# Optimization experiments

Hardware: AMD Instinct MI355X
Metric: run time of the kernel (lower is better)

Reference implementation:

```python
import jax, jax.numpy as jnp
import numpy as np

HIDDEN = 1024
HEADS = 16
HEAD_DIM = HIDDEN // HEADS
EPS = 1e-6


def _layernorm(x, gamma, beta):
    mu = jnp.mean(x, axis=-1, keepdims=True)
    var = jnp.mean(jnp.square(x - mu), axis=-1, keepdims=True)
    return (x - mu) * jax.lax.rsqrt(var + EPS) * gamma + beta


def setup_inputs() -> dict:
    key = jax.random.key(0)
    ks = jax.random.split(key, 16)
    B, S, D = 2, 2048, HIDDEN
    s = 1.0 / np.sqrt(D)
    inp = {
        "x": jax.random.normal(ks[0], (B, S, D), dtype=jnp.float32),
        "Wq": jax.random.uniform(ks[1], (D, D), jnp.float32, -s, s),
        "bq": jnp.zeros((D,), jnp.float32),
        "Wk": jax.random.uniform(ks[2], (D, D), jnp.float32, -s, s),
        "bk": jnp.zeros((D,), jnp.float32),
        "Wv": jax.random.uniform(ks[3], (D, D), jnp.float32, -s, s),
        "bv": jnp.zeros((D,), jnp.float32),
        "Wo": jax.random.uniform(ks[4], (D, D), jnp.float32, -s, s),
        "bo": jnp.zeros((D,), jnp.float32),
        "g1": jnp.ones((D,), jnp.float32),
        "b1": jnp.zeros((D,), jnp.float32),
        "Wup": jax.random.uniform(ks[5], (D, 4 * D), jnp.float32, -s, s),
        "bup": jnp.zeros((4 * D,), jnp.float32),
        "Wdn": jax.random.uniform(ks[6], (4 * D, D), jnp.float32, -0.5 * s, 0.5 * s),
        "bdn": jnp.zeros((D,), jnp.float32),
        "g2": jnp.ones((D,), jnp.float32),
        "b2": jnp.zeros((D,), jnp.float32),
    }
    return inp


def _forward(x, Wq, bq, Wk, bk, Wv, bv, Wo, bo, g1, b1, Wup, bup, Wdn, bdn, g2, b2):
    B, S, D = x.shape
    H, Hd = HEADS, HEAD_DIM
    # projections -> (B, H, S, Hd)
    q = (x @ Wq + bq).reshape(B, S, H, Hd).transpose(0, 2, 1, 3)
    k = (x @ Wk + bk).reshape(B, S, H, Hd).transpose(0, 2, 1, 3)
    v = (x @ Wv + bv).reshape(B, S, H, Hd).transpose(0, 2, 1, 3)
    # full NxN scores (faithful to the source: explicit QK^T, mask, softmax, AV)
    scores = jnp.einsum("bhqd,bhkd->bhqk", q, k) / np.sqrt(Hd)
    causal = jnp.tril(jnp.ones((S, S), dtype=bool))  # (S, S)
    scores = jnp.where(causal, scores, jnp.float32(-1e20))
    attn = jax.nn.softmax(scores, axis=-1)
    # dropout is identity in eval mode
    mid = jnp.einsum("bhqk,bhkd->bqhd", attn, v).reshape(B, S, D)
    attn_out = mid @ Wo + bo
    x = _layernorm(x + attn_out, g1, b1)
    # FFN
    up = jax.nn.relu(x @ Wup + bup)
    down = up @ Wdn + bdn
    return _layernorm(x + down, g2, b2)


def reference(x, Wq, bq, Wk, bk, Wv, bv, Wo, bo, g1, b1, Wup, bup, Wdn, bdn, g2, b2):
    return _forward(x, Wq, bq, Wk, bk, Wv, bv, Wo, bo, g1, b1, Wup, bup, Wdn, bdn, g2, b2)
```

## Files before the change

kernel.cpp:

```cpp
#include <hip/hip_runtime.h>

#define D_MODEL 1024
#define D_FFN   4096
#define SEQ     2048
#define NROWS   4096
#define QKV_LD  3072
#define BKG     64

typedef __bf16 bf16x8 __attribute__((ext_vector_type(8)));
typedef float  floatx4 __attribute__((ext_vector_type(4)));

__device__ __forceinline__ unsigned short f2bf(float f) {
  unsigned int u = __float_as_uint(f);
  u += 0x7FFFu + ((u >> 16) & 1u);
  return (unsigned short)(u >> 16);
}

template <int C>
__device__ __forceinline__ float ror16(float x) {
  return __int_as_float(
      __builtin_amdgcn_mov_dpp(__float_as_int(x), 0x120 | C, 0xf, 0xf, true));
}

__device__ __forceinline__ void async16(const unsigned short* g, unsigned short* l) {
  __builtin_amdgcn_global_load_lds(
      (const __attribute__((address_space(1))) unsigned int*)g,
      (__attribute__((address_space(3))) unsigned int*)l, 16, 0, 0);
}

__global__ __launch_bounds__(256) void k_f32_to_bf16(
    const float* __restrict__ in, unsigned short* __restrict__ outp, long n) {
  long i = ((long)blockIdx.x * 256 + threadIdx.x) * 4;
  if (i >= n) return;
  float4 v = *(const float4*)(in + i);
  ushort4 o;
  o.x = f2bf(v.x); o.y = f2bf(v.y); o.z = f2bf(v.z); o.w = f2bf(v.w);
  *(ushort4*)(outp + i) = o;
}

__global__ __launch_bounds__(256) void k_transpose_bf16(
    const float* __restrict__ W, unsigned short* __restrict__ WT, int R, int C) {
  __shared__ float tile[32][33];
  int tx = threadIdx.x & 31, ty = threadIdx.x >> 5;
  long bx = (long)blockIdx.x * 32;
  long by = (long)blockIdx.y * 32;
  #pragma unroll
  for (int j = 0; j < 4; j++)
    tile[ty + j * 8][tx] = W[(by + ty + j * 8) * C + bx + tx];
  __syncthreads();
  #pragma unroll
  for (int j = 0; j < 4; j++)
    WT[(bx + ty + j * 8) * R + by + tx] = f2bf(tile[tx][ty + j * 8]);
}

__global__ __launch_bounds__(256) void k_transpose_sq(
    const float* __restrict__ Wq, const float* __restrict__ Wk,
    const float* __restrict__ Wv, const float* __restrict__ Wo,
    unsigned short* __restrict__ WqkvT, unsigned short* __restrict__ WoT) {
  __shared__ float tile[32][33];
  int z = blockIdx.z;
  const float* W = (z == 0) ? Wq : (z == 1) ? Wk : (z == 2) ? Wv : Wo;
  unsigned short* dst = (z < 3) ? (WqkvT + (size_t)z * D_MODEL * D_MODEL) : WoT;
  int tx = threadIdx.x & 31, ty = threadIdx.x >> 5;
  long bx = (long)blockIdx.x * 32;
  long by = (long)blockIdx.y * 32;
  #pragma unroll
  for (int j = 0; j < 4; j++)
    tile[ty + j * 8][tx] = W[(by + ty + j * 8) * D_MODEL + bx + tx];
  __syncthreads();
  #pragma unroll
  for (int j = 0; j < 4; j++)
    dst[(bx + ty + j * 8) * D_MODEL + by + tx] = f2bf(tile[tx][ty + j * 8]);
}

__global__ __launch_bounds__(256) void k_pack_bias(
    const float* __restrict__ bq, const float* __restrict__ bk,
    const float* __restrict__ bv, float* __restrict__ dst) {
  int i = blockIdx.x * 256 + threadIdx.x;
  if (i >= 3072) return;
  float v = (i < 1024) ? bq[i] : (i < 2048) ? bk[i - 1024] : bv[i - 2048];
  dst[i] = v;
}

__global__ __launch_bounds__(256) void k_transpose_v(
    const unsigned short* __restrict__ QKV, unsigned short* __restrict__ Vt) {
  __shared__ unsigned short tile[64][72];
  int r0 = blockIdx.x * 64;
  int c0 = blockIdx.y * 64;
  int tx = threadIdx.x & 15, ty = threadIdx.x >> 4;
  #pragma unroll
  for (int j = 0; j < 4; j++) {
    int r = ty + j * 16;
    *(ushort4*)&tile[r][tx * 4] =
        *(const ushort4*)(QKV + (long)(r0 + r) * QKV_LD + 2048 + c0 + tx * 4);
  }
  __syncthreads();
  #pragma unroll
  for (int j = 0; j < 4; j++) {
    int d = ty + j * 16;
    ushort4 o;
    o.x = tile[tx * 4 + 0][d];
    o.y = tile[tx * 4 + 1][d];
    o.z = tile[tx * 4 + 2][d];
    o.w = tile[tx * 4 + 3][d];
    *(ushort4*)(Vt + (long)(c0 + d) * NROWS + r0 + tx * 4) = o;
  }
}

__global__ __launch_bounds__(256) void k_gemm(
    const unsigned short* __restrict__ A,
    const unsigned short* __restrict__ Bt,
    const float* __restrict__ bias,
    void* __restrict__ Cp, int M, int N, int K, int flags) {
  __shared__ unsigned short As[128 * BKG];
  __shared__ unsigned short Bs[128 * BKG];
  int tid = threadIdx.x, lane = tid & 63, wave = tid >> 6;
  int quad = lane >> 4, l16 = lane & 15;
  int wm = (wave & 1) * 64, wn = (wave >> 1) * 64;
  long bm = (long)blockIdx.x * 128;
  long bn = (long)blockIdx.y * 128;
  int nz = gridDim.z, z = blockIdx.z;
  int Ks = K / nz;
  long zb = (long)z * Ks;

  const floatx4 fz = {0.f, 0.f, 0.f, 0.f};
  floatx4 acc[4][4];
  #pragma unroll
  for (int i = 0; i < 4; i++)
    #pragma unroll
    for (int j = 0; j < 4; j++) acc[i][j] = fz;

  int srow = lane >> 3;
  int sc = (lane & 7) ^ srow;
  const unsigned short* Ag = A + (bm + wave * 8 + srow) * (long)K + zb + sc * 8;
  const unsigned short* Bg = Bt + (bn + wave * 8 + srow) * (long)K + zb + sc * 8;
  unsigned short* Asw = As + wave * 8 * BKG;
  unsigned short* Bsw = Bs + wave * 8 * BKG;

  for (int k0 = 0; k0 < Ks; k0 += BKG) {
    #pragma unroll
    for (int j = 0; j < 4; j++) {
      async16(Ag + (long)j * 32 * K + k0, Asw + j * 32 * BKG);
      async16(Bg + (long)j * 32 * K + k0, Bsw + j * 32 * BKG);
    }
    __syncthreads();
    bf16x8 af[4][2], bfr[4][2];
    #pragma unroll
    for (int i = 0; i < 4; i++) {
      int r = wm + i * 16 + l16;
      int sw = r & 7;
      af[i][0] = *(const bf16x8*)(As + r * BKG + (quad ^ sw) * 8);
      af[i][1] = *(const bf16x8*)(As + r * BKG + ((4 + quad) ^ sw) * 8);
    }
    #pragma unroll
    for (int j = 0; j < 4; j++) {
      int r = wn + j * 16 + l16;
      int sw = r & 7;
      bfr[j][0] = *(const bf16x8*)(Bs + r * BKG + (quad ^ sw) * 8);
      bfr[j][1] = *(const bf16x8*)(Bs + r * BKG + ((4 + quad) ^ sw) * 8);
    }
    #pragma unroll
    for (int h = 0; h < 2; h++)
      #pragma unroll
      for (int i = 0; i < 4; i++)
        #pragma unroll
        for (int j = 0; j < 4; j++)
          acc[i][j] = __builtin_amdgcn_mfma_f32_16x16x32_bf16(af[i][h], bfr[j][h],
                                                             acc[i][j], 0, 0, 0);
    __syncthreads();
  }

  bool f32out = (flags & 1) != 0;
  bool relu   = (flags & 2) != 0;
  float* outf = (float*)Cp + (size_t)z * M * (size_t)N;
  #pragma unroll
  for (int j = 0; j < 4; j++) {
    long col = bn + wn + j * 16 + l16;
    float bvv = (z == 0) ? bias[col] : 0.0f;
    #pragma unroll
    for (int i = 0; i < 4; i++) {
      long row = bm + wm + i * 16 + quad * 4;
      #pragma unroll
      for (int r = 0; r < 4; r++) {
        float v = acc[i][j][r] + bvv;
        if (relu) v = fmaxf(v, 0.0f);
        if (f32out) outf[(row + r) * (long)N + col] = v;
        else        ((unsigned short*)Cp)[(row + r) * (long)N + col] = f2bf(v);
      }
    }
  }
}

#define PLD 72
__global__ __launch_bounds__(256) void k_attn(
    const unsigned short* __restrict__ QKV,
    const unsigned short* __restrict__ Vt,
    unsigned short* __restrict__ Omat) {
  __shared__ unsigned short Ks[64 * 64];
  __shared__ unsigned short Vs[64 * 64];
  __shared__ unsigned short Ps[4][16 * PLD];
  int tid = threadIdx.x;
  int lane = tid & 63, wave = tid >> 6;
  int quad = lane >> 4, l16 = lane & 15;
  int z = blockIdx.x;
  int bh = z & 31;
  int qp = z >> 5;
  int b = bh >> 4, h = bh & 15;
  long rowbase = (long)b * SEQ;
  int hd0 = h * 64;
  unsigned short* pw = &Ps[wave][0];
  const float SCL = 0.18033688f;
  const floatx4 fz = {0.f, 0.f, 0.f, 0.f};

  int r_in = lane >> 3;
  int cpos = lane & 7;

  bf16x8 ones;
  #pragma unroll
  for (int i = 0; i < 8; i++) ones[i] = (__bf16)1.0f;

  #pragma unroll
  for (int phase = 0; phase < 2; phase++) {
    int qt = phase ? qp : (31 - qp);
    int q0w = qt * 64 + wave * 16;
    int qrow = q0w + quad * 4;
    int ntiles = qt + 1;

    bf16x8 qf0, qf1;
    {
      const unsigned short* qp_ =
          QKV + (rowbase + q0w + l16) * (long)QKV_LD + hd0 + quad * 8;
      qf0 = *(const bf16x8*)(qp_);
      qf1 = *(const bf16x8*)(qp_ + 32);
    }

    floatx4 ao[4], aol;
    #pragma unroll
    for (int t = 0; t < 4; t++) ao[t] = fz;
    aol = fz;
    float m_i[4];
    #pragma unroll
    for (int r = 0; r < 4; r++) m_i[r] = -3.0e38f;

    for (int it = 0; it < ntiles; it++) {
      int kv0 = it << 6;
      #pragma unroll
      for (int jj = 0; jj < 2; jj++) {
        int j = wave * 2 + jj;
        int r = j * 8 + r_in;
        int c = cpos ^ (r & 7);
        const unsigned short* gk =
            QKV + (rowbase + kv0 + r) * (long)QKV_LD + 1024 + hd0 + c * 8;
        async16(gk, Ks + j * 512);
        const unsigned short* gv =
            Vt + (long)(hd0 + r) * NROWS + rowbase + kv0 + c * 8;
        async16(gv, Vs + j * 512);
      }
      __syncthreads();

      floatx4 sacc[4];
      #pragma unroll
      for (int t = 0; t < 4; t++) {
        int row = t * 16 + l16;
        int sw = row & 7;
        bf16x8 kf0 = *(const bf16x8*)(Ks + row * 64 + (quad ^ sw) * 8);
        bf16x8 kf1 = *(const bf16x8*)(Ks + row * 64 + ((quad + 4) ^ sw) * 8);
        sacc[t] = __builtin_amdgcn_mfma_f32_16x16x32_bf16(qf0, kf0, fz, 0, 0, 0);
        sacc[t] = __builtin_amdgcn_mfma_f32_16x16x32_bf16(qf1, kf1, sacc[t], 0, 0, 0);
      }

      bool maskt = (it == ntiles - 1);
      if (maskt) {
        #pragma unroll
        for (int t = 0; t < 4; t++) {
          int kvc = kv0 + t * 16 + l16;
          #pragma unroll
          for (int r = 0; r < 4; r++) {
            float s = sacc[t][r] * SCL;
            sacc[t][r] = (kvc > qrow + r) ? -1.0e30f : s;
          }
        }
      } else {
        #pragma unroll
        for (int t = 0; t < 4; t++)
          #pragma unroll
          for (int r = 0; r < 4; r++) sacc[t][r] *= SCL;
      }

      float Mg = sacc[0][0];
      #pragma unroll
      for (int t = 0; t < 4; t++)
        #pragma unroll
        for (int r = 0; r < 4; r++) Mg = fmaxf(Mg, sacc[t][r]);
      Mg = fmaxf(Mg, ror16<1>(Mg));
      Mg = fmaxf(Mg, ror16<2>(Mg));
      Mg = fmaxf(Mg, ror16<4>(Mg));
      Mg = fmaxf(Mg, ror16<8>(Mg));

      float alpha[4];
      #pragma unroll
      for (int r = 0; r < 4; r++) {
        float mn = fmaxf(m_i[r], Mg);
        alpha[r] = __builtin_amdgcn_exp2f(m_i[r] - mn);
        m_i[r] = mn;
      }

      #pragma unroll
      for (int t = 0; t < 4; t++)
        #pragma unroll
        for (int r = 0; r < 4; r++) {
          float p = __builtin_amdgcn_exp2f(sacc[t][r] - m_i[r]);
          pw[(quad * 4 + r) * PLD + t * 16 + l16] =
              (unsigned short)(__float_as_uint(p) >> 16);
        }

      #pragma unroll
      for (int t = 0; t < 4; t++)
        #pragma unroll
        for (int r = 0; r < 4; r++) ao[t][r] *= alpha[r];
      #pragma unroll
      for (int r = 0; r < 4; r++) aol[r] *= alpha[r];

      __asm__ volatile("s_waitcnt lgkmcnt(0)" ::: "memory");
      bf16x8 pf0 = *(const bf16x8*)(pw + l16 * PLD + quad * 8);
      bf16x8 pf1 = *(const bf16x8*)(pw + l16 * PLD + 32 + quad * 8);

      #pragma unroll
      for (int t = 0; t < 4; t++) {
        int row = t * 16 + l16;
        int sw = row & 7;
        bf16x8 vf0 = *(const bf16x8*)(Vs + row * 64 + (quad ^ sw) * 8);
        bf16x8 vf1 = *(const bf16x8*)(Vs + row * 64 + ((quad + 4) ^ sw) * 8);
        ao[t] = __builtin_amdgcn_mfma_f32_16x16x32_bf16(pf0, vf0, ao[t], 0, 0, 0);
        ao[t] = __builtin_amdgcn_mfma_f32_16x16x32_bf16(pf1, vf1, ao[t], 0, 0, 0);
      }
      aol = __builtin_amdgcn_mfma_f32_16x16x32_bf16(pf0, ones, aol, 0, 0, 0);
      aol = __builtin_amdgcn_mfma_f32_16x16x32_bf16(pf1, ones, aol, 0, 0, 0);

      __syncthreads();
    }

    float inv[4];
    #pragma unroll
    for (int r = 0; r < 4; r++) inv[r] = 1.0f / aol[r];
    #pragma unroll
    for (int t = 0; t < 4; t++)
      #pragma unroll
      for (int r = 0; r < 4; r++)
        Omat[(rowbase + qrow + r) * (long)D_MODEL + hd0 + t * 16 + l16] =
            f2bf(ao[t][r] * inv[r]);
  }
}

__global__ __launch_bounds__(256) void k_add_ln(
    const float* __restrict__ A, const float* __restrict__ R1,
    const float* __restrict__ R2,
    const float* __restrict__ g, const float* __restrict__ be,
    float* __restrict__ Y, unsigned short* __restrict__ Ybf) {
  __shared__ float sb[4], ssb[4];
  int tid = threadIdx.x;
  long base = (long)blockIdx.x * D_MODEL + tid * 4;
  float4 a  = *(const float4*)(A + base);
  float4 r1 = *(const float4*)(R1 + base);
  float4 r2 = *(const float4*)(R2 + base);
  float v0 = a.x + r1.x + r2.x, v1 = a.y + r1.y + r2.y;
  float v2 = a.z + r1.z + r2.z, v3 = a.w + r1.w + r2.w;
  float s  = v0 + v1 + v2 + v3;
  float ss = v0 * v0 + v1 * v1 + v2 * v2 + v3 * v3;
  #pragma unroll
  for (int o = 32; o >= 1; o >>= 1) {
    s  += __shfl_xor(s, o, 64);
    ss += __shfl_xor(ss, o, 64);
  }
  int wave = tid >> 6;
  if ((tid & 63) == 0) { sb[wave] = s; ssb[wave] = ss; }
  __syncthreads();
  s  = sb[0] + sb[1] + sb[2] + sb[3];
  ss = ssb[0] + ssb[1] + ssb[2] + ssb[3];
  float mu  = s * (1.0f / 1024.0f);
  float var = ss * (1.0f / 1024.0f) - mu * mu;
  float rstd = rsqrtf(var + 1e-6f);
  float4 gv  = *(const float4*)(g + tid * 4);
  float4 bev = *(const float4*)(be + tid * 4);
  float o0 = (v0 - mu) * rstd * gv.x + bev.x;
  float o1 = (v1 - mu) * rstd * gv.y + bev.y;
  float o2 = (v2 - mu) * rstd * gv.z + bev.z;
  float o3 = (v3 - mu) * rstd * gv.w + bev.w;
  if (Y) *(float4*)(Y + base) = make_float4(o0, o1, o2, o3);
  if (Ybf) {
    ushort4 u;
    u.x = f2bf(o0); u.y = f2bf(o1); u.z = f2bf(o2); u.w = f2bf(o3);
    *(ushort4*)(Ybf + base) = u;
  }
}

extern "C" void kernel_launch(void* const* d_in, const int* in_sizes, int n_in,
                              void* d_out, int out_size, void* d_ws, size_t ws_size,
                              hipStream_t stream) {
  (void)in_sizes; (void)n_in; (void)out_size; (void)ws_size;
  const float* x   = (const float*)d_in[0];
  const float* Wq  = (const float*)d_in[1];
  const float* bq  = (const float*)d_in[2];
  const float* Wk  = (const float*)d_in[3];
  const float* bk  = (const float*)d_in[4];
  const float* Wv  = (const float*)d_in[5];
  const float* bv  = (const float*)d_in[6];
  const float* Wo  = (const float*)d_in[7];
  const float* bo  = (const float*)d_in[8];
  const float* g1  = (const float*)d_in[9];
  const float* b1  = (const float*)d_in[10];
  const float* Wup = (const float*)d_in[11];
  const float* bup = (const float*)d_in[12];
  const float* Wdn = (const float*)d_in[13];
  const float* bdn = (const float*)d_in[14];
  const float* g2  = (const float*)d_in[15];
  const float* b2  = (const float*)d_in[16];
  float* out = (float*)d_out;

  char* ws = (char*)d_ws;
  size_t off = 0;
  auto alloc = [&](size_t bytes) {
    char* p = ws + off;
    off = (off + bytes + 255) & ~(size_t)255;
    return p;
  };
  unsigned short* x_bf   = (unsigned short*)alloc((size_t)NROWS * D_MODEL * 2);
  unsigned short* WqkvT  = (unsigned short*)alloc((size_t)QKV_LD * D_MODEL * 2);
  unsigned short* WoT    = (unsigned short*)alloc((size_t)D_MODEL * D_MODEL * 2);
  unsigned short* WupT   = (unsigned short*)alloc((size_t)D_FFN * D_MODEL * 2);
  unsigned short* WdnT   = (unsigned short*)alloc((size_t)D_MODEL * D_FFN * 2);
  float*          bqkv   = (float*)alloc((size_t)QKV_LD * 4);
  unsigned short* qkv_bf = (unsigned short*)alloc((size_t)NROWS * QKV_LD * 2);
  unsigned short* Vt     = (unsigned short*)alloc((size_t)D_MODEL * NROWS * 2);
  unsigned short* mid_bf = (unsigned short*)alloc((size_t)NROWS * D_MODEL * 2);
  float*          x1f    = (float*)alloc((size_t)NROWS * D_MODEL * 4);
  unsigned short* x1bf   = (unsigned short*)alloc((size_t)NROWS * D_MODEL * 2);
  float*          part   = (float*)alloc((size_t)2 * NROWS * D_MODEL * 4);
  unsigned short* h_bf   = (unsigned short*)alloc((size_t)NROWS * D_FFN * 2);
  float*          part1  = part + (size_t)NROWS * D_MODEL;

  k_f32_to_bf16<<<4096, 256, 0, stream>>>(x, x_bf, (long)NROWS * D_MODEL);
  k_transpose_sq<<<dim3(32, 32, 4), 256, 0, stream>>>(Wq, Wk, Wv, Wo, WqkvT, WoT);
  k_transpose_bf16<<<dim3(128, 32), 256, 0, stream>>>(Wup, WupT, D_MODEL, D_FFN);
  k_transpose_bf16<<<dim3(32, 128), 256, 0, stream>>>(Wdn, WdnT, D_FFN, D_MODEL);
  k_pack_bias<<<12, 256, 0, stream>>>(bq, bk, bv, bqkv);

  k_gemm<<<dim3(32, 24), 256, 0, stream>>>(x_bf, WqkvT, bqkv, qkv_bf,
                                           NROWS, QKV_LD, D_MODEL, 0);
  k_transpose_v<<<dim3(64, 16), 256, 0, stream>>>(qkv_bf, Vt);

  k_attn<<<512, 256, 0, stream>>>(qkv_bf, Vt, mid_bf);

  k_gemm<<<dim3(32, 8, 2), 256, 0, stream>>>(mid_bf, WoT, bo, part,
                                             NROWS, D_MODEL, D_MODEL, 1);
  k_add_ln<<<4096, 256, 0, stream>>>(x, part, part1, g1, b1, x1f, x1bf);

  k_gemm<<<dim3(32, 32), 256, 0, stream>>>(x1bf, WupT, bup, h_bf,
                                           NROWS, D_FFN, D_MODEL, 2);
  k_gemm<<<dim3(32, 8, 2), 256, 0, stream>>>(h_bf, WdnT, bdn, part,
                                             NROWS, D_MODEL, D_FFN, 1);
  k_add_ln<<<4096, 256, 0, stream>>>(x1f, part, part1, g2, b2, out, nullptr);
}
```

Before: 395.1 us.

## Double-buffer GEMM K tiles and raise split-K to four partials

The GEMM kernel now uses two 32-wide K stages in shared memory and issues async loads for the next stage before computing the current one, with a single barrier per iteration. The output and down projections use four-way split-K, and the add-layernorm kernel sums a variable number of partial buffers. The partial buffer aliases the dead qkv and transposed-V workspace. This hides global load latency and adds parallelism, at the cost of more barriers per K and extra partial-sum memory traffic.

Result: slower. 412.5 us (+4.4%).

```diff
diff --git a/kernel.cpp b/kernel.cpp
--- a/kernel.cpp
+++ b/kernel.cpp
@@ -5,7 +5,6 @@
 #define SEQ     2048
 #define NROWS   4096
 #define QKV_LD  3072
-#define BKG     64
 
 typedef __bf16 bf16x8 __attribute__((ext_vector_type(8)));
 typedef float  floatx4 __attribute__((ext_vector_type(4)));
@@ -112,8 +111,8 @@
     const unsigned short* __restrict__ Bt,
     const float* __restrict__ bias,
     void* __restrict__ Cp, int M, int N, int K, int flags) {
-  __shared__ unsigned short As[128 * BKG];
-  __shared__ unsigned short Bs[128 * BKG];
+  __shared__ unsigned short As[2][128 * 32];
+  __shared__ unsigned short Bs[2][128 * 32];
   int tid = threadIdx.x, lane = tid & 63, wave = tid >> 6;
   int quad = lane >> 4, l16 = lane & 15;
   int wm = (wave & 1) * 64, wn = (wave >> 1) * 64;
@@ -130,44 +129,41 @@
     #pragma unroll
     for (int j = 0; j < 4; j++) acc[i][j] = fz;
 
-  int srow = lane >> 3;
-  int sc = (lane & 7) ^ srow;
-  const unsigned short* Ag = A + (bm + wave * 8 + srow) * (long)K + zb + sc * 8;
-  const unsigned short* Bg = Bt + (bn + wave * 8 + srow) * (long)K + zb + sc * 8;
-  unsigned short* Asw = As + wave * 8 * BKG;
-  unsigned short* Bsw = Bs + wave * 8 * BKG;
-
-  for (int k0 = 0; k0 < Ks; k0 += BKG) {
-    #pragma unroll
-    for (int j = 0; j < 4; j++) {
-      async16(Ag + (long)j * 32 * K + k0, Asw + j * 32 * BKG);
-      async16(Bg + (long)j * 32 * K + k0, Bsw + j * 32 * BKG);
-    }
+  int srow = lane >> 2;
+  int c0 = (lane & 3) ^ (srow & 3);
+  int r0 = wave * 16 + srow;
+  const unsigned short* Ag = A + (bm + r0) * (long)K + zb + c0 * 8;
+  const unsigned short* Bg = Bt + (bn + r0) * (long)K + zb + c0 * 8;
+
+  auto stage = [&](int b, int k0) {
+    async16(Ag + k0, As[b] + (wave * 16) * 32);
+    async16(Ag + (long)64 * K + k0, As[b] + (wave * 16 + 64) * 32);
+    async16(Bg + k0, Bs[b] + (wave * 16) * 32);
+    async16(Bg + (long)64 * K + k0, Bs[b] + (wave * 16 + 64) * 32);
+  };
+
+  stage(0, 0);
+  int cur = 0;
+  for (int k0 = 0; k0 < Ks; k0 += 32) {
     __syncthreads();
-    bf16x8 af[4][2], bfr[4][2];
+    if (k0 + 32 < Ks) stage(cur ^ 1, k0 + 32);
+    bf16x8 af[4], bfr[4];
     #pragma unroll
     for (int i = 0; i < 4; i++) {
       int r = wm + i * 16 + l16;
-      int sw = r & 7;
-      af[i][0] = *(const bf16x8*)(As + r * BKG + (quad ^ sw) * 8);
-      af[i][1] = *(const bf16x8*)(As + r * BKG + ((4 + quad) ^ sw) * 8);
+      af[i] = *(const bf16x8*)(As[cur] + r * 32 + (quad ^ (r & 3)) * 8);
     }
     #pragma unroll
     for (int j = 0; j < 4; j++) {
       int r = wn + j * 16 + l16;
-      int sw = r & 7;
-      bfr[j][0] = *(const bf16x8*)(Bs + r * BKG + (quad ^ sw) * 8);
-      bfr[j][1] = *(const bf16x8*)(Bs + r * BKG + ((4 + quad) ^ sw) * 8);
+      bfr[j] = *(const bf16x8*)(Bs[cur] + r * 32 + (quad ^ (r & 3)) * 8);
     }
     #pragma unroll
-    for (int h = 0; h < 2; h++)
-      #pragma unroll
-      for (int i = 0; i < 4; i++)
-        #pragma unroll
-        for (int j = 0; j < 4; j++)
-          acc[i][j] = __builtin_amdgcn_mfma_f32_16x16x32_bf16(af[i][h], bfr[j][h],
-                                                             acc[i][j], 0, 0, 0);
-    __syncthreads();
+    for (int i = 0; i < 4; i++)
+      #pragma unroll
+      for (int j = 0; j < 4; j++)
+        acc[i][j] = __builtin_amdgcn_mfma_f32_16x16x32_bf16(af[i], bfr[j], acc[i][j], 0, 0, 0);
+    cur ^= 1;
   }
 
   bool f32out = (flags & 1) != 0;
@@ -353,18 +349,19 @@
 }
 
 __global__ __launch_bounds__(256) void k_add_ln(
-    const float* __restrict__ A, const float* __restrict__ R1,
-    const float* __restrict__ R2,
+    const float* __restrict__ A, const float* __restrict__ P, int np,
     const float* __restrict__ g, const float* __restrict__ be,
     float* __restrict__ Y, unsigned short* __restrict__ Ybf) {
   __shared__ float sb[4], ssb[4];
   int tid = threadIdx.x;
   long base = (long)blockIdx.x * D_MODEL + tid * 4;
-  float4 a  = *(const float4*)(A + base);
-  float4 r1 = *(const float4*)(R1 + base);
-  float4 r2 = *(const float4*)(R2 + base);
-  float v0 = a.x + r1.x + r2.x, v1 = a.y + r1.y + r2.y;
-  float v2 = a.z + r1.z + r2.z, v3 = a.w + r1.w + r2.w;
+  float4 a = *(const float4*)(A + base);
+  float v0 = a.x, v1 = a.y, v2 = a.z, v3 = a.w;
+  #pragma unroll 4
+  for (int p = 0; p < np; p++) {
+    float4 r = *(const float4*)(P + (size_t)p * NROWS * D_MODEL + base);
+    v0 += r.x; v1 += r.y; v2 += r.z; v3 += r.w;
+  }
   float s  = v0 + v1 + v2 + v3;
   float ss = v0 * v0 + v1 * v1 + v2 * v2 + v3 * v3;
   #pragma unroll
@@ -430,14 +427,13 @@
   unsigned short* WupT   = (unsigned short*)alloc((size_t)D_FFN * D_MODEL * 2);
   unsigned short* WdnT   = (unsigned short*)alloc((size_t)D_MODEL * D_FFN * 2);
   float*          bqkv   = (float*)alloc((size_t)QKV_LD * 4);
-  unsigned short* qkv_bf = (unsigned short*)alloc((size_t)NROWS * QKV_LD * 2);
-  unsigned short* Vt     = (unsigned short*)alloc((size_t)D_MODEL * NROWS * 2);
-  unsigned short* mid_bf = (unsigned short*)alloc((size_t)NROWS * D_MODEL * 2);
   float*          x1f    = (float*)alloc((size_t)NROWS * D_MODEL * 4);
   unsigned short* x1bf   = (unsigned short*)alloc((size_t)NROWS * D_MODEL * 2);
-  float*          part   = (float*)alloc((size_t)2 * NROWS * D_MODEL * 4);
+  float*          R      = (float*)alloc((size_t)4 * NROWS * D_MODEL * 4);
+  unsigned short* qkv_bf = (unsigned short*)R;
+  unsigned short* Vt     = (unsigned short*)((char*)R + (size_t)NROWS * QKV_LD * 2);
+  unsigned short* mid_bf = (unsigned short*)alloc((size_t)NROWS * D_MODEL * 2);
   unsigned short* h_bf   = (unsigned short*)alloc((size_t)NROWS * D_FFN * 2);
-  float*          part1  = part + (size_t)NROWS * D_MODEL;
 
   k_f32_to_bf16<<<4096, 256, 0, stream>>>(x, x_bf, (long)NROWS * D_MODEL);
   k_transpose_sq<<<dim3(32, 32, 4), 256, 0, stream>>>(Wq, Wk, Wv, Wo, WqkvT, WoT);
@@ -451,13 +447,13 @@
 
   k_attn<<<512, 256, 0, stream>>>(qkv_bf, Vt, mid_bf);
 
-  k_gemm<<<dim3(32, 8, 2), 256, 0, stream>>>(mid_bf, WoT, bo, part,
+  k_gemm<<<dim3(32, 8, 4), 256, 0, stream>>>(mid_bf, WoT, bo, R,
                                              NROWS, D_MODEL, D_MODEL, 1);
-  k_add_ln<<<4096, 256, 0, stream>>>(x, part, part1, g1, b1, x1f, x1bf);
+  k_add_ln<<<4096, 256, 0, stream>>>(x, R, 4, g1, b1, x1f, x1bf);
 
   k_gemm<<<dim3(32, 32), 256, 0, stream>>>(x1bf, WupT, bup, h_bf,
                                            NROWS, D_FFN, D_MODEL, 2);
-  k_gemm<<<dim3(32, 8, 2), 256, 0, stream>>>(h_bf, WdnT, bdn, part,
+  k_gemm<<<dim3(32, 8, 4), 256, 0, stream>>>(h_bf, WdnT, bdn, R,
                                              NROWS, D_MODEL, D_FFN, 1);
-  k_add_ln<<<4096, 256, 0, stream>>>(x1f, part, part1, g2, b2, out, nullptr);
-}
+  k_add_ln<<<4096, 256, 0, stream>>>(x1f, R, 4, g2, b2, out, nullptr);
+}
```
